# Performance work log

Measured on AMD Instinct MI355X. Metric: run time of the kernel, lower is better.

The kernel has to match this reference:

```python
import jax, jax.numpy as jnp
import numpy as np

SCALE = 8.0  # sqrt(d_k), d_k = 64
NEG_INF = -1000000000.0


def setup_inputs() -> dict:
    key = jax.random.key(0)
    ks = jax.random.split(key, 7)
    B, H, S, D = 2, 8, 4096, 64
    shp = (B, H, S, D)
    q_a = jax.random.normal(ks[0], shp, dtype=jnp.float32)
    k_a = jax.random.normal(ks[1], shp, dtype=jnp.float32)
    v_a = jax.random.normal(ks[2], shp, dtype=jnp.float32)
    q_s = jax.random.normal(ks[3], shp, dtype=jnp.float32)
    k_s = jax.random.normal(ks[4], shp, dtype=jnp.float32)
    v_s = jax.random.normal(ks[5], shp, dtype=jnp.float32)
    mask = jax.random.randint(ks[6], (B, 1, 1, S), 0, 2, dtype=jnp.int32)
    return {"q_a": q_a, "k_a": k_a, "v_a": v_a,
            "q_s": q_s, "k_s": k_s, "v_s": v_s, "mask": mask}


def reference(q_a, k_a, v_a, q_s, k_s, v_s, mask):
    # a2a + a2s + s2a + s2s == (q_a + q_s) @ (k_a + k_s)^T  (exact algebra)
    q = q_a + q_s                               # [B,H,S,D]
    k = k_a + k_s                               # [B,H,S,D]
    score = jnp.einsum("bhqd,bhkd->bhqk", q, k) / SCALE  # [B,H,S,S]
    score = jnp.where(mask == 0, NEG_INF, score)
    attn = jax.nn.softmax(score, axis=-1)       # dropout p=0 (eval/identity)
    out = jnp.einsum("bhqk,bhkd->bhqd", attn, v_a + v_s)
    return out
```

## Files before the change

kernel.cpp:

```cpp
#include <hip/hip_runtime.h>
#include <hip/hip_bf16.h>

#define S_   4096
#define D_   64
#define BH_  16
#define QW   64
#define QBLK 256
#define KVB  128
#define NCH  2

typedef __attribute__((ext_vector_type(8)))  short short8_t;
typedef __attribute__((ext_vector_type(16))) float f32x16;
#define QSCALE 0.18033688011112042f

__device__ __forceinline__ unsigned short f2bf(float f) {
  unsigned u = __float_as_uint(f);
  u += 0x7fffu + ((u >> 16) & 1u);
  return (unsigned short)(u >> 16);
}

__device__ __forceinline__ void glds16(const unsigned short* g, unsigned short* l) {
  __builtin_amdgcn_global_load_lds(
      (const __attribute__((address_space(1))) unsigned int*)g,
      (__attribute__((address_space(3))) unsigned int*)l, 16, 0, 0);
}

__global__ void kvgather_kernel(const float* __restrict__ ka, const float* __restrict__ ks,
                                const float* __restrict__ va, const float* __restrict__ vs,
                                const float* __restrict__ qa, const float* __restrict__ qs,
                                const int* __restrict__ mask, int* __restrict__ cnt,
                                unsigned short* __restrict__ qhat,
                                unsigned short* __restrict__ khat,
                                unsigned short* __restrict__ vt) {
  __shared__ int ps[256];
  __shared__ int srcLds[64];
  __shared__ __align__(16) unsigned short t[D_][72];
  const int bh = blockIdx.y, b = bh >> 3;
  const int s0 = blockIdx.x * 64;
  const int tid = threadIdx.x;

  const int* mb = mask + (size_t)b * S_;
  int m[16], c = 0;
  const int base = tid * 16;
#pragma unroll
  for (int i = 0; i < 16; ++i) { m[i] = mb[base + i]; c += (m[i] != 0); }
  ps[tid] = c;
  __syncthreads();
  for (int off = 1; off < 256; off <<= 1) {
    int add = (tid >= off) ? ps[tid - off] : 0;
    __syncthreads();
    ps[tid] += add;
    __syncthreads();
  }
  const int C = ps[255];
  int pos = ps[tid] - c;
#pragma unroll
  for (int i = 0; i < 16; ++i) {
    if (m[i]) {
      int r = pos++;
      if (r >= s0 && r < s0 + 64) srcLds[r - s0] = base + i;
    }
  }
  if (tid == 0 && blockIdx.x == 0 && (bh & 7) == 0) cnt[b] = C;
  __syncthreads();

  const int row16 = tid >> 4;
  const int col4  = (tid & 15) * 4;
#pragma unroll
  for (int p = 0; p < 4; ++p) {
    int srow = p * 16 + row16;
    int j = s0 + srow;
    {
      size_t qoff = ((size_t)bh * S_ + j) * D_ + col4;
      float4 xq = *(const float4*)(qa + qoff);
      float4 yq = *(const float4*)(qs + qoff);
      ushort4 rq;
      rq.x = f2bf((xq.x + yq.x) * QSCALE); rq.y = f2bf((xq.y + yq.y) * QSCALE);
      rq.z = f2bf((xq.z + yq.z) * QSCALE); rq.w = f2bf((xq.w + yq.w) * QSCALE);
      *(ushort4*)(qhat + qoff) = rq;
    }
    float4 xv = {0, 0, 0, 0}, yv = {0, 0, 0, 0};
    float4 xk = {0, 0, 0, 0}, yk = {0, 0, 0, 0};
    if (j < C) {
      int src = srcLds[srow];
      size_t off = ((size_t)bh * S_ + src) * D_ + col4;
      xv = *(const float4*)(va + off);
      yv = *(const float4*)(vs + off);
      xk = *(const float4*)(ka + off);
      yk = *(const float4*)(ks + off);
    }
    t[col4 + 0][srow] = f2bf(xv.x + yv.x);
    t[col4 + 1][srow] = f2bf(xv.y + yv.y);
    t[col4 + 2][srow] = f2bf(xv.z + yv.z);
    t[col4 + 3][srow] = f2bf(xv.w + yv.w);
    ushort4 rk;
    rk.x = f2bf(xk.x + yk.x); rk.y = f2bf(xk.y + yk.y);
    rk.z = f2bf(xk.z + yk.z); rk.w = f2bf(xk.w + yk.w);
    *(ushort4*)(khat + ((size_t)bh * S_ + j) * D_ + col4) = rk;
  }
  __syncthreads();
#pragma unroll
  for (int r = 0; r < 2; ++r) {
    int e = (r * 256 + tid) * 8;
    int d = e >> 6, sc = e & 63;
    short8_t v = *(const short8_t*)&t[d][sc];
    *(short8_t*)(vt + ((size_t)bh * D_ + d) * S_ + s0 + sc) = v;
  }
}

__global__ __launch_bounds__(256, 2) void attn_kernel(
    const unsigned short* __restrict__ Qb, const unsigned short* __restrict__ Kb,
    const unsigned short* __restrict__ Vt, const int* __restrict__ cnt,
    float* __restrict__ out, float* __restrict__ Opar, float2* __restrict__ Ml) {
  __shared__ __align__(16) unsigned short lK[2][KVB * 64];
  __shared__ __align__(16) unsigned short lV[2][64 * KVB];

  const int tid  = threadIdx.x;
  const int wave = tid >> 6;
  const int lane = tid & 63;
  const int l31  = lane & 31;
  const int h5   = lane >> 5;
  const int rsw  = l31 & 7;
  const int bh   = blockIdx.y;
  const int ch   = blockIdx.z;
  const int qrow0 = blockIdx.x * QBLK + wave * QW + l31;
  const int b    = bh >> 3;
  const int C    = cnt[b];
  const int NTt  = (C + KVB - 1) / KVB;
  const int tpc  = (NTt + NCH - 1) / NCH;
  const int ts   = ch * tpc;
  const int te   = (ts + tpc < NTt) ? (ts + tpc) : NTt;

  short8_t qf[2][4];
#pragma unroll
  for (int qb = 0; qb < 2; ++qb) {
    const unsigned short* qp = Qb + ((size_t)bh * S_ + qrow0 + 32 * qb) * D_ + h5 * 8;
#pragma unroll
    for (int t4 = 0; t4 < 4; ++t4) qf[qb][t4] = *(const short8_t*)(qp + t4 * 16);
  }

  short8_t ones8;
#pragma unroll
  for (int i = 0; i < 8; ++i) ones8[i] = (short)0x3F80;

  const unsigned short* gk0 = Kb + (size_t)bh * S_ * D_;
  const unsigned short* gv0 = Vt + (size_t)bh * D_ * S_;

  int srcK[4], srcV[4], ldsB[4];
#pragma unroll
  for (int r2 = 0; r2 < 4; ++r2) {
    int c = r2 * 256 + tid;
    int rowK = c >> 3, gK = (c & 7) ^ (rowK & 7);
    srcK[r2] = rowK * 64 + gK * 8;
    int rowV = c >> 4, gg = c & 15;
    int swg = (gg & 8) | ((gg & 7) ^ (rowV & 7));
    srcV[r2] = rowV * S_ + swg * 8;
    ldsB[r2] = r2 * 2048 + wave * 512;
  }

  f32x16 acc0[2], acc1[2], accS[2];
  float mrow[2];
#pragma unroll
  for (int qb = 0; qb < 2; ++qb) {
    acc0[qb] = (f32x16)(0.0f); acc1[qb] = (f32x16)(0.0f); accS[qb] = (f32x16)(0.0f);
    mrow[qb] = -1e30f;
  }

  if (ts < te) {
#pragma unroll
    for (int r2 = 0; r2 < 4; ++r2) {
      glds16(gk0 + (size_t)ts * KVB * D_ + srcK[r2], &lK[0][ldsB[r2]]);
      glds16(gv0 + ts * KVB + srcV[r2], &lV[0][ldsB[r2]]);
    }

    for (int t = ts; t < te; ++t) {
      const int cur = (t - ts) & 1;
      if (t + 1 < te) {
#pragma unroll
        for (int r2 = 0; r2 < 4; ++r2) {
          glds16(gk0 + (size_t)(t + 1) * KVB * D_ + srcK[r2], &lK[cur ^ 1][ldsB[r2]]);
          glds16(gv0 + (t + 1) * KVB + srcV[r2], &lV[cur ^ 1][ldsB[r2]]);
        }
        asm volatile("s_waitcnt vmcnt(8)" ::: "memory");
      } else {
        asm volatile("s_waitcnt vmcnt(0)" ::: "memory");
      }
      __builtin_amdgcn_s_barrier();
      __builtin_amdgcn_sched_barrier(0);

#pragma unroll
      for (int h = 0; h < 2; ++h) {
        f32x16 sv0[2], sv1[2];
#pragma unroll
        for (int qb = 0; qb < 2; ++qb) { sv0[qb] = (f32x16)(0.0f); sv1[qb] = (f32x16)(0.0f); }
        __builtin_amdgcn_s_setprio(1);
#pragma unroll
        for (int t4 = 0; t4 < 4; ++t4) {
          int g = ((2 * t4 + h5) ^ rsw) * 8;
          short8_t kf0 = *(const short8_t*)&lK[cur][(h * 64 + l31) * 64 + g];
          short8_t kf1 = *(const short8_t*)&lK[cur][(h * 64 + 32 + l31) * 64 + g];
          sv0[0] = __builtin_amdgcn_mfma_f32_32x32x16_bf16(kf0, qf[0][t4], sv0[0], 0, 0, 0);
          sv0[1] = __builtin_amdgcn_mfma_f32_32x32x16_bf16(kf0, qf[1][t4], sv0[1], 0, 0, 0);
          sv1[0] = __builtin_amdgcn_mfma_f32_32x32x16_bf16(kf1, qf[0][t4], sv1[0], 0, 0, 0);
          sv1[1] = __builtin_amdgcn_mfma_f32_32x32x16_bf16(kf1, qf[1][t4], sv1[1], 0, 0, 0);
        }
        __builtin_amdgcn_s_setprio(0);

        if (t == NTt - 1) {
          int kvb = t * KVB + h * 64;
#pragma unroll
          for (int i = 0; i < 16; ++i) {
            int key = kvb + (i & 3) + 8 * (i >> 2) + 4 * h5;
#pragma unroll
            for (int qb = 0; qb < 2; ++qb) {
              if (key >= C) sv0[qb][i] = -1e9f;
              if (key + 32 >= C) sv1[qb][i] = -1e9f;
            }
          }
        }

        unsigned int pkw[2][16];
#pragma unroll
        for (int qb = 0; qb < 2; ++qb) {
          float tmx[8];
#pragma unroll
          for (int i = 0; i < 8; ++i)
            tmx[i] = fmaxf(fmaxf(sv0[qb][i], sv0[qb][i + 8]),
                           fmaxf(sv1[qb][i], sv1[qb][i + 8]));
#pragma unroll
          for (int i = 0; i < 4; ++i) tmx[i] = fmaxf(tmx[i], tmx[i + 4]);
          float tm = fmaxf(fmaxf(tmx[0], tmx[1]), fmaxf(tmx[2], tmx[3]));
          tm = fmaxf(tm, __shfl_xor(tm, 32));

          if (__any(tm > mrow[qb] + 8.0f)) {
            float mnew = fmaxf(mrow[qb], tm);
            float sc = __builtin_amdgcn_exp2f(mrow[qb] - mnew);
            mrow[qb] = mnew;
            accS[qb][0] *= sc;
#pragma unroll
            for (int i = 0; i < 16; ++i) { acc0[qb][i] *= sc; acc1[qb][i] *= sc; }
          }

          float m = mrow[qb];
#pragma unroll
          for (int i = 0; i < 16; i += 4) {
            sv0[qb][i + 0] = __builtin_amdgcn_exp2f(sv0[qb][i + 0] - m);
            sv0[qb][i + 1] = __builtin_amdgcn_exp2f(sv0[qb][i + 1] - m);
            sv0[qb][i + 2] = __builtin_amdgcn_exp2f(sv0[qb][i + 2] - m);
            sv0[qb][i + 3] = __builtin_amdgcn_exp2f(sv0[qb][i + 3] - m);
            sv1[qb][i + 0] = __builtin_amdgcn_exp2f(sv1[qb][i + 0] - m);
            sv1[qb][i + 1] = __builtin_amdgcn_exp2f(sv1[qb][i + 1] - m);
            sv1[qb][i + 2] = __builtin_amdgcn_exp2f(sv1[qb][i + 2] - m);
            sv1[qb][i + 3] = __builtin_amdgcn_exp2f(sv1[qb][i + 3] - m);
          }

#pragma unroll
          for (int rg = 0; rg < 4; ++rg) {
            __hip_bfloat162 a0 = __float22bfloat162_rn({sv0[qb][rg * 4 + 0], sv0[qb][rg * 4 + 1]});
            __hip_bfloat162 a1 = __float22bfloat162_rn({sv0[qb][rg * 4 + 2], sv0[qb][rg * 4 + 3]});
            __hip_bfloat162 b0 = __float22bfloat162_rn({sv1[qb][rg * 4 + 0], sv1[qb][rg * 4 + 1]});
            __hip_bfloat162 b1 = __float22bfloat162_rn({sv1[qb][rg * 4 + 2], sv1[qb][rg * 4 + 3]});
            pkw[qb][rg * 2 + 0] = *(unsigned int*)&a0;
            pkw[qb][rg * 2 + 1] = *(unsigned int*)&a1;
            pkw[qb][8 + rg * 2 + 0] = *(unsigned int*)&b0;
            pkw[qb][8 + rg * 2 + 1] = *(unsigned int*)&b1;
          }
        }

        __builtin_amdgcn_s_setprio(1);
#pragma unroll
        for (int kt = 0; kt < 4; ++kt) {
          const int n = kt >> 1, k1 = kt & 1;
          int gcol = ((h * 8) | ((2 * kt + h5) ^ rsw)) * 8;
          short8_t vf0 = *(const short8_t*)&lV[cur][l31 * KVB + gcol];
          short8_t vf1 = *(const short8_t*)&lV[cur][(32 + l31) * KVB + gcol];
#pragma unroll
          for (int qb = 0; qb < 2; ++qb) {
            unsigned int sA = pkw[qb][n * 8 + (2 * k1 + h5) * 2 + 0];
            unsigned int sB = pkw[qb][n * 8 + (2 * k1 + h5) * 2 + 1];
            unsigned int xA = pkw[qb][n * 8 + (2 * k1 + (h5 ^ 1)) * 2 + 0];
            unsigned int xB = pkw[qb][n * 8 + (2 * k1 + (h5 ^ 1)) * 2 + 1];
            unsigned int pA = (unsigned int)__shfl_xor((int)xA, 32);
            unsigned int pB = (unsigned int)__shfl_xor((int)xB, 32);
            union { unsigned int u[4]; short8_t v; } bb;
            bb.u[0] = h5 ? pA : sA;
            bb.u[1] = h5 ? pB : sB;
            bb.u[2] = h5 ? sA : pA;
            bb.u[3] = h5 ? sB : pB;
            acc0[qb] = __builtin_amdgcn_mfma_f32_32x32x16_bf16(vf0, bb.v, acc0[qb], 0, 0, 0);
            acc1[qb] = __builtin_amdgcn_mfma_f32_32x32x16_bf16(vf1, bb.v, acc1[qb], 0, 0, 0);
            accS[qb] = __builtin_amdgcn_mfma_f32_32x32x16_bf16(ones8, bb.v, accS[qb], 0, 0, 0);
          }
        }
        __builtin_amdgcn_s_setprio(0);
      }

      __builtin_amdgcn_sched_barrier(0);
      __builtin_amdgcn_s_barrier();
    }
  }

  float* Op = (ch == 0) ? out : Opar;
#pragma unroll
  for (int qb = 0; qb < 2; ++qb) {
    float* op = Op + ((size_t)bh * S_ + qrow0 + 32 * qb) * D_;
#pragma unroll
    for (int rg = 0; rg < 4; ++rg) {
      float4 o0, o1;
      o0.x = acc0[qb][rg * 4 + 0]; o0.y = acc0[qb][rg * 4 + 1];
      o0.z = acc0[qb][rg * 4 + 2]; o0.w = acc0[qb][rg * 4 + 3];
      o1.x = acc1[qb][rg * 4 + 0]; o1.y = acc1[qb][rg * 4 + 1];
      o1.z = acc1[qb][rg * 4 + 2]; o1.w = acc1[qb][rg * 4 + 3];
      *(float4*)(op + rg * 8 + h5 * 4) = o0;
      *(float4*)(op + 32 + rg * 8 + h5 * 4) = o1;
    }
    if (h5 == 0) {
      float2 st; st.x = mrow[qb]; st.y = accS[qb][0];
      Ml[(size_t)ch * (BH_ * S_) + (size_t)bh * S_ + qrow0 + 32 * qb] = st;
    }
  }
}

__global__ void combine_kernel(const float* __restrict__ O1, const float2* __restrict__ Ml,
                               float* __restrict__ out) {
  int gid = blockIdx.x * 256 + threadIdx.x;
  int row = gid >> 2, qd = (gid & 3) * 16;
  float2 a = Ml[row];
  float2 b = Ml[BH_ * S_ + row];
  float M = fmaxf(a.x, b.x);
  float w0 = exp2f(a.x - M), w1 = exp2f(b.x - M);
  float inv = 1.0f / (a.y * w0 + b.y * w1);
  w0 *= inv; w1 *= inv;
  const float4* p0 = (const float4*)(out + (size_t)row * D_ + qd);
  const float4* p1 = (const float4*)(O1 + (size_t)row * D_ + qd);
  float4* po = (float4*)(out + (size_t)row * D_ + qd);
#pragma unroll
  for (int i = 0; i < 4; ++i) {
    float4 x = p0[i], y = p1[i];
    float4 r;
    r.x = x.x * w0 + y.x * w1; r.y = x.y * w0 + y.y * w1;
    r.z = x.z * w0 + y.z * w1; r.w = x.w * w0 + y.w * w1;
    po[i] = r;
  }
}

extern "C" void kernel_launch(void* const* d_in, const int* in_sizes, int n_in,
                              void* d_out, int out_size, void* d_ws, size_t ws_size,
                              hipStream_t stream) {
  const float* q_a = (const float*)d_in[0];
  const float* k_a = (const float*)d_in[1];
  const float* v_a = (const float*)d_in[2];
  const float* q_s = (const float*)d_in[3];
  const float* k_s = (const float*)d_in[4];
  const float* v_s = (const float*)d_in[5];
  const int*   mask = (const int*)d_in[6];
  float* out = (float*)d_out;
  (void)in_sizes; (void)n_in; (void)out_size; (void)ws_size;

  const int N = BH_ * S_ * D_;
  unsigned short* qhat = (unsigned short*)d_ws;
  unsigned short* khat = qhat + N;
  unsigned short* vt   = khat + N;
  int*  cnt  = (int*)(vt + N);
  float* O1  = (float*)(cnt + 4);
  float2* ml = (float2*)(O1 + N);

  {
    dim3 g(S_ / 64, BH_);
    kvgather_kernel<<<g, 256, 0, stream>>>(k_a, k_s, v_a, v_s, q_a, q_s, mask, cnt,
                                           qhat, khat, vt);
  }
  {
    dim3 g(S_ / QBLK, BH_, NCH);
    attn_kernel<<<g, 256, 0, stream>>>(qhat, khat, vt, cnt, out, O1, ml);
  }
  combine_kernel<<<(BH_ * S_ * 4) / 256, 256, 0, stream>>>(O1, ml, out);
}
```

Measured before the change: 119.2 us.

## Merge split-KV halves within one 512-thread block and combine via LDS

Result: faster. 109.3 us, median of 2 (-8.3%).

```diff
diff --git a/kernel.cpp b/kernel.cpp
--- a/kernel.cpp
+++ b/kernel.cpp
@@ -108,27 +108,30 @@
   }
 }
 
-__global__ __launch_bounds__(256, 2) void attn_kernel(
+__global__ __launch_bounds__(512, 1) void attn_kernel(
     const unsigned short* __restrict__ Qb, const unsigned short* __restrict__ Kb,
     const unsigned short* __restrict__ Vt, const int* __restrict__ cnt,
-    float* __restrict__ out, float* __restrict__ Opar, float2* __restrict__ Ml) {
-  __shared__ __align__(16) unsigned short lK[2][KVB * 64];
-  __shared__ __align__(16) unsigned short lV[2][64 * KVB];
+    float* __restrict__ out) {
+  __shared__ __align__(16) unsigned char smem[131072];
+  unsigned short* lKp = (unsigned short*)smem;
+  unsigned short* lVp = lKp + 32768;
 
   const int tid  = threadIdx.x;
   const int wave = tid >> 6;
+  const int chid = wave >> 2;
+  const int wq   = wave & 3;
+  const int ctid = tid & 255;
   const int lane = tid & 63;
   const int l31  = lane & 31;
   const int h5   = lane >> 5;
   const int rsw  = l31 & 7;
   const int bh   = blockIdx.y;
-  const int ch   = blockIdx.z;
-  const int qrow0 = blockIdx.x * QBLK + wave * QW + l31;
+  const int qrow0 = blockIdx.x * QBLK + wq * QW + l31;
   const int b    = bh >> 3;
   const int C    = cnt[b];
   const int NTt  = (C + KVB - 1) / KVB;
   const int tpc  = (NTt + NCH - 1) / NCH;
-  const int ts   = ch * tpc;
+  const int ts   = chid * tpc;
   const int te   = (ts + tpc < NTt) ? (ts + tpc) : NTt;
 
   short8_t qf[2][4];
@@ -149,14 +152,16 @@
   int srcK[4], srcV[4], ldsB[4];
 #pragma unroll
   for (int r2 = 0; r2 < 4; ++r2) {
-    int c = r2 * 256 + tid;
+    int c = r2 * 256 + ctid;
     int rowK = c >> 3, gK = (c & 7) ^ (rowK & 7);
     srcK[r2] = rowK * 64 + gK * 8;
     int rowV = c >> 4, gg = c & 15;
     int swg = (gg & 8) | ((gg & 7) ^ (rowV & 7));
     srcV[r2] = rowV * S_ + swg * 8;
-    ldsB[r2] = r2 * 2048 + wave * 512;
-  }
+    ldsB[r2] = r2 * 2048 + wq * 512;
+  }
+  unsigned short* lK0 = lKp + chid * 2 * 8192;
+  unsigned short* lV0 = lVp + chid * 2 * 8192;
 
   f32x16 acc0[2], acc1[2], accS[2];
   float mrow[2];
@@ -169,25 +174,30 @@
   if (ts < te) {
 #pragma unroll
     for (int r2 = 0; r2 < 4; ++r2) {
-      glds16(gk0 + (size_t)ts * KVB * D_ + srcK[r2], &lK[0][ldsB[r2]]);
-      glds16(gv0 + ts * KVB + srcV[r2], &lV[0][ldsB[r2]]);
-    }
-
-    for (int t = ts; t < te; ++t) {
-      const int cur = (t - ts) & 1;
-      if (t + 1 < te) {
-#pragma unroll
-        for (int r2 = 0; r2 < 4; ++r2) {
-          glds16(gk0 + (size_t)(t + 1) * KVB * D_ + srcK[r2], &lK[cur ^ 1][ldsB[r2]]);
-          glds16(gv0 + (t + 1) * KVB + srcV[r2], &lV[cur ^ 1][ldsB[r2]]);
-        }
-        asm volatile("s_waitcnt vmcnt(8)" ::: "memory");
-      } else {
-        asm volatile("s_waitcnt vmcnt(0)" ::: "memory");
+      glds16(gk0 + (size_t)ts * KVB * D_ + srcK[r2], lK0 + ldsB[r2]);
+      glds16(gv0 + ts * KVB + srcV[r2], lV0 + ldsB[r2]);
+    }
+  }
+
+  for (int it = 0; it < tpc; ++it) {
+    const int t = ts + it;
+    const int cur = it & 1;
+    if (t + 1 < te) {
+#pragma unroll
+      for (int r2 = 0; r2 < 4; ++r2) {
+        glds16(gk0 + (size_t)(t + 1) * KVB * D_ + srcK[r2], lK0 + (cur ^ 1) * 8192 + ldsB[r2]);
+        glds16(gv0 + (t + 1) * KVB + srcV[r2], lV0 + (cur ^ 1) * 8192 + ldsB[r2]);
       }
-      __builtin_amdgcn_s_barrier();
-      __builtin_amdgcn_sched_barrier(0);
-
+      asm volatile("s_waitcnt vmcnt(8)" ::: "memory");
+    } else {
+      asm volatile("s_waitcnt vmcnt(0)" ::: "memory");
+    }
+    __builtin_amdgcn_s_barrier();
+    __builtin_amdgcn_sched_barrier(0);
+
+    if (t < te) {
+      const unsigned short* lK = lK0 + cur * 8192;
+      const unsigned short* lV = lV0 + cur * 8192;
 #pragma unroll
       for (int h = 0; h < 2; ++h) {
         f32x16 sv0[2], sv1[2];
@@ -197,8 +207,8 @@
 #pragma unroll
         for (int t4 = 0; t4 < 4; ++t4) {
           int g = ((2 * t4 + h5) ^ rsw) * 8;
-          short8_t kf0 = *(const short8_t*)&lK[cur][(h * 64 + l31) * 64 + g];
-          short8_t kf1 = *(const short8_t*)&lK[cur][(h * 64 + 32 + l31) * 64 + g];
+          short8_t kf0 = *(const short8_t*)&lK[(h * 64 + l31) * 64 + g];
+          short8_t kf1 = *(const short8_t*)&lK[(h * 64 + 32 + l31) * 64 + g];
           sv0[0] = __builtin_amdgcn_mfma_f32_32x32x16_bf16(kf0, qf[0][t4], sv0[0], 0, 0, 0);
           sv0[1] = __builtin_amdgcn_mfma_f32_32x32x16_bf16(kf0, qf[1][t4], sv0[1], 0, 0, 0);
           sv1[0] = __builtin_amdgcn_mfma_f32_32x32x16_bf16(kf1, qf[0][t4], sv1[0], 0, 0, 0);
@@ -272,8 +282,8 @@
         for (int kt = 0; kt < 4; ++kt) {
           const int n = kt >> 1, k1 = kt & 1;
           int gcol = ((h * 8) | ((2 * kt + h5) ^ rsw)) * 8;
-          short8_t vf0 = *(const short8_t*)&lV[cur][l31 * KVB + gcol];
-          short8_t vf1 = *(const short8_t*)&lV[cur][(32 + l31) * KVB + gcol];
+          short8_t vf0 = *(const short8_t*)&lV[l31 * KVB + gcol];
+          short8_t vf1 = *(const short8_t*)&lV[(32 + l31) * KVB + gcol];
 #pragma unroll
           for (int qb = 0; qb < 2; ++qb) {
             unsigned int sA = pkw[qb][n * 8 + (2 * k1 + h5) * 2 + 0];
@@ -294,53 +304,64 @@
         }
         __builtin_amdgcn_s_setprio(0);
       }
-
-      __builtin_amdgcn_sched_barrier(0);
-      __builtin_amdgcn_s_barrier();
-    }
-  }
-
-  float* Op = (ch == 0) ? out : Opar;
-#pragma unroll
-  for (int qb = 0; qb < 2; ++qb) {
-    float* op = Op + ((size_t)bh * S_ + qrow0 + 32 * qb) * D_;
-#pragma unroll
-    for (int rg = 0; rg < 4; ++rg) {
-      float4 o0, o1;
-      o0.x = acc0[qb][rg * 4 + 0]; o0.y = acc0[qb][rg * 4 + 1];
-      o0.z = acc0[qb][rg * 4 + 2]; o0.w = acc0[qb][rg * 4 + 3];
-      o1.x = acc1[qb][rg * 4 + 0]; o1.y = acc1[qb][rg * 4 + 1];
-      o1.z = acc1[qb][rg * 4 + 2]; o1.w = acc1[qb][rg * 4 + 3];
-      *(float4*)(op + rg * 8 + h5 * 4) = o0;
-      *(float4*)(op + 32 + rg * 8 + h5 * 4) = o1;
-    }
-    if (h5 == 0) {
-      float2 st; st.x = mrow[qb]; st.y = accS[qb][0];
-      Ml[(size_t)ch * (BH_ * S_) + (size_t)bh * S_ + qrow0 + 32 * qb] = st;
-    }
-  }
-}
-
-__global__ void combine_kernel(const float* __restrict__ O1, const float2* __restrict__ Ml,
-                               float* __restrict__ out) {
-  int gid = blockIdx.x * 256 + threadIdx.x;
-  int row = gid >> 2, qd = (gid & 3) * 16;
-  float2 a = Ml[row];
-  float2 b = Ml[BH_ * S_ + row];
-  float M = fmaxf(a.x, b.x);
-  float w0 = exp2f(a.x - M), w1 = exp2f(b.x - M);
-  float inv = 1.0f / (a.y * w0 + b.y * w1);
-  w0 *= inv; w1 *= inv;
-  const float4* p0 = (const float4*)(out + (size_t)row * D_ + qd);
-  const float4* p1 = (const float4*)(O1 + (size_t)row * D_ + qd);
-  float4* po = (float4*)(out + (size_t)row * D_ + qd);
-#pragma unroll
-  for (int i = 0; i < 4; ++i) {
-    float4 x = p0[i], y = p1[i];
-    float4 r;
-    r.x = x.x * w0 + y.x * w1; r.y = x.y * w0 + y.y * w1;
-    r.z = x.z * w0 + y.z * w1; r.w = x.w * w0 + y.w * w1;
-    po[i] = r;
+    }
+
+    __builtin_amdgcn_sched_barrier(0);
+    __builtin_amdgcn_s_barrier();
+  }
+
+  float* part = (float*)smem;
+  float2* mlsh = (float2*)(smem + 73728);
+  __syncthreads();
+
+  if (chid == 1) {
+#pragma unroll
+    for (int qb = 0; qb < 2; ++qb) {
+      int rl = wq * 64 + qb * 32 + l31;
+      float* pr = part + rl * 72;
+#pragma unroll
+      for (int rg = 0; rg < 4; ++rg) {
+        float4 o0, o1;
+        o0.x = acc0[qb][rg * 4 + 0]; o0.y = acc0[qb][rg * 4 + 1];
+        o0.z = acc0[qb][rg * 4 + 2]; o0.w = acc0[qb][rg * 4 + 3];
+        o1.x = acc1[qb][rg * 4 + 0]; o1.y = acc1[qb][rg * 4 + 1];
+        o1.z = acc1[qb][rg * 4 + 2]; o1.w = acc1[qb][rg * 4 + 3];
+        *(float4*)(pr + rg * 8 + h5 * 4) = o0;
+        *(float4*)(pr + 32 + rg * 8 + h5 * 4) = o1;
+      }
+      if (h5 == 0) { float2 st; st.x = mrow[qb]; st.y = accS[qb][0]; mlsh[rl] = st; }
+    }
+  }
+  __syncthreads();
+  if (chid == 0) {
+#pragma unroll
+    for (int qb = 0; qb < 2; ++qb) {
+      int rl = wq * 64 + qb * 32 + l31;
+      float2 pml = mlsh[rl];
+      float m0 = mrow[qb], l0 = accS[qb][0];
+      float M = fmaxf(m0, pml.x);
+      float w0 = exp2f(m0 - M), w1 = exp2f(pml.x - M);
+      float inv = 1.0f / (l0 * w0 + pml.y * w1);
+      w0 *= inv; w1 *= inv;
+      const float* pr = part + rl * 72;
+      float* op = out + ((size_t)bh * S_ + qrow0 + 32 * qb) * D_;
+#pragma unroll
+      for (int rg = 0; rg < 4; ++rg) {
+        float4 p0v = *(const float4*)(pr + rg * 8 + h5 * 4);
+        float4 p1v = *(const float4*)(pr + 32 + rg * 8 + h5 * 4);
+        float4 o0, o1;
+        o0.x = acc0[qb][rg * 4 + 0] * w0 + p0v.x * w1;
+        o0.y = acc0[qb][rg * 4 + 1] * w0 + p0v.y * w1;
+        o0.z = acc0[qb][rg * 4 + 2] * w0 + p0v.z * w1;
+        o0.w = acc0[qb][rg * 4 + 3] * w0 + p0v.w * w1;
+        o1.x = acc1[qb][rg * 4 + 0] * w0 + p1v.x * w1;
+        o1.y = acc1[qb][rg * 4 + 1] * w0 + p1v.y * w1;
+        o1.z = acc1[qb][rg * 4 + 2] * w0 + p1v.z * w1;
+        o1.w = acc1[qb][rg * 4 + 3] * w0 + p1v.w * w1;
+        *(float4*)(op + rg * 8 + h5 * 4) = o0;
+        *(float4*)(op + 32 + rg * 8 + h5 * 4) = o1;
+      }
+    }
   }
 }
 
@@ -361,9 +382,7 @@
   unsigned short* qhat = (unsigned short*)d_ws;
   unsigned short* khat = qhat + N;
   unsigned short* vt   = khat + N;
-  int*  cnt  = (int*)(vt + N);
-  float* O1  = (float*)(cnt + 4);
-  float2* ml = (float2*)(O1 + N);
+  int* cnt = (int*)(vt + N);
 
   {
     dim3 g(S_ / 64, BH_);
@@ -371,8 +390,7 @@
                                            qhat, khat, vt);
   }
   {
-    dim3 g(S_ / QBLK, BH_, NCH);
-    attn_kernel<<<g, 256, 0, stream>>>(qhat, khat, vt, cnt, out, O1, ml);
-  }
-  combine_kernel<<<(BH_ * S_ * 4) / 256, 256, 0, stream>>>(O1, ml, out);
-}
+    dim3 g(S_ / QBLK, BH_);
+    attn_kernel<<<g, 512, 0, stream>>>(qhat, khat, vt, cnt, out);
+  }
+}
```
